# Kernel tuning notes

Measured on AMD Instinct MI355X. Metric: run time of the kernel, lower is better.

Reference implementation:

```python
import jax, jax.numpy as jnp
import numpy as np

N_FEATURES = 4096
N_GROUPS = 1024
BATCH = 8192


def _make_groups():
    # Deterministic variable-size groups: size_g = 2 + (g % 7), sizes in [2, 8].
    rng = np.random.RandomState(0)
    sizes = 2 + (np.arange(N_GROUPS) % 7)
    flat_idx = rng.randint(0, N_FEATURES, size=int(sizes.sum())).astype(np.int64)
    seg_ids = np.repeat(np.arange(N_GROUPS, dtype=np.int64), sizes)
    return flat_idx, seg_ids


def setup_inputs() -> dict:
    key = jax.random.key(0)
    k1, k2, k3, k4 = jax.random.split(key, 4)
    flat_idx_np, seg_ids_np = _make_groups()
    total = flat_idx_np.shape[0]  # 5115
    x = jax.random.normal(k1, (BATCH, N_FEATURES), dtype=jnp.float32)
    # Concatenated per-group HeNormal-style weights (shape (size,1) flattened).
    w_flat = jax.random.normal(k2, (total,), dtype=jnp.float32)
    # SimplyConnected weight (Ones init in original; random here for testing).
    diag_w = jax.random.uniform(k3, (N_GROUPS,), dtype=jnp.float32)
    # Dense kernel [n_groups, units=1], no bias.
    dense_W = jax.random.normal(k4, (N_GROUPS, 1), dtype=jnp.float32) * (2.0 / N_GROUPS) ** 0.5
    return {
        "x": x,
        "flat_idx": jnp.asarray(flat_idx_np),
        "seg_ids": jnp.asarray(seg_ids_np),
        "w_flat": w_flat,
        "diag_w": diag_w,
        "dense_W": dense_W,
    }


def reference(x, flat_idx, seg_ids, w_flat, diag_w, dense_W):
    # GroupConnected: per-group gather + (size,1) matmul == segmented weighted sum.
    # gathered: [B, total_idx]; weighted then segment-summed over groups -> [B, n_groups]
    weighted = x[:, flat_idx] * w_flat  # [B, total]
    grouped = jax.ops.segment_sum(weighted.T, seg_ids, num_segments=N_GROUPS).T  # [B, G]
    # diagblock (depth-2 = 1 SimplyConnected): elementwise scale, then Dense (no bias).
    return (grouped * diag_w) @ dense_W  # [B, units=1]
```

## Files before the change

kernel.cpp:

```cpp
#include <hip/hip_runtime.h>

#define N_FEATURES 4096
#define N_GROUPS   1024
#define BATCH      8192
#define NV4        (N_FEATURES / 4)

__global__ __launch_bounds__(1024) void build_coeff_kernel(
    const int* __restrict__ flat_idx,
    const int* __restrict__ seg_ids,
    const float* __restrict__ w_flat,
    const float* __restrict__ diag_w,
    const float* __restrict__ dense_W,
    float* __restrict__ coeff,
    int total)
{
    __shared__ float s_coeff[N_FEATURES];
    for (int i = threadIdx.x; i < N_FEATURES; i += blockDim.x) s_coeff[i] = 0.0f;
    __syncthreads();
    for (int i = threadIdx.x; i < total; i += blockDim.x) {
        int g = seg_ids[i];
        float c = w_flat[i] * diag_w[g] * dense_W[g];
        atomicAdd(&s_coeff[flat_idx[i]], c);
    }
    __syncthreads();
    for (int i = threadIdx.x; i < N_FEATURES; i += blockDim.x) coeff[i] = s_coeff[i];
}

__global__ __launch_bounds__(256) void gemv_kernel(
    const float* __restrict__ x,
    const float* __restrict__ coeff,
    float* __restrict__ out)
{
    __shared__ float4 s_c[NV4];
    const float4* __restrict__ c4 = (const float4*)coeff;
    for (int i = threadIdx.x; i < NV4; i += 256) s_c[i] = c4[i];
    __syncthreads();

    const int wid  = threadIdx.x >> 6;
    const int lane = threadIdx.x & 63;
    const int row  = (blockIdx.x << 2) + wid;

    const float4* __restrict__ xr = (const float4*)(x + (size_t)row * N_FEATURES);

    float acc = 0.0f;
#pragma unroll
    for (int k = 0; k < 16; ++k) {
        const int i = (k << 6) + lane;
        float4 xv = xr[i];
        float4 cv = s_c[i];
        acc += xv.x * cv.x + xv.y * cv.y + xv.z * cv.z + xv.w * cv.w;
    }

#pragma unroll
    for (int off = 32; off > 0; off >>= 1)
        acc += __shfl_down(acc, off, 64);

    if (lane == 0)
        out[row] = acc;
}

extern "C" void kernel_launch(void* const* d_in, const int* in_sizes, int n_in,
                              void* d_out, int out_size, void* d_ws, size_t ws_size,
                              hipStream_t stream) {
    const float* x        = (const float*)d_in[0];
    const int*   flat_idx = (const int*)d_in[1];
    const int*   seg_ids  = (const int*)d_in[2];
    const float* w_flat   = (const float*)d_in[3];
    const float* diag_w   = (const float*)d_in[4];
    const float* dense_W  = (const float*)d_in[5];
    float* out = (float*)d_out;
    const int total = in_sizes[1];

    float* coeff = (float*)d_ws;

    build_coeff_kernel<<<1, 1024, 0, stream>>>(flat_idx, seg_ids, w_flat,
                                               diag_w, dense_W, coeff, total);
    gemv_kernel<<<BATCH / 4, 256, 0, stream>>>(x, coeff, out);
}
```

Before: 206.5 us.

## Fuse coefficient build into GEMV and prefetch x rows before building

```diff
diff --git a/kernel.cpp b/kernel.cpp
--- a/kernel.cpp
+++ b/kernel.cpp
@@ -5,50 +5,43 @@
 #define BATCH      8192
 #define NV4        (N_FEATURES / 4)
 
-__global__ __launch_bounds__(1024) void build_coeff_kernel(
+__global__ __launch_bounds__(256) void fused_kernel(
+    const float* __restrict__ x,
     const int* __restrict__ flat_idx,
     const int* __restrict__ seg_ids,
     const float* __restrict__ w_flat,
     const float* __restrict__ diag_w,
     const float* __restrict__ dense_W,
-    float* __restrict__ coeff,
+    float* __restrict__ out,
     int total)
 {
     __shared__ float s_coeff[N_FEATURES];
-    for (int i = threadIdx.x; i < N_FEATURES; i += blockDim.x) s_coeff[i] = 0.0f;
-    __syncthreads();
-    for (int i = threadIdx.x; i < total; i += blockDim.x) {
-        int g = seg_ids[i];
-        float c = w_flat[i] * diag_w[g] * dense_W[g];
-        atomicAdd(&s_coeff[flat_idx[i]], c);
-    }
-    __syncthreads();
-    for (int i = threadIdx.x; i < N_FEATURES; i += blockDim.x) coeff[i] = s_coeff[i];
-}
-
-__global__ __launch_bounds__(256) void gemv_kernel(
-    const float* __restrict__ x,
-    const float* __restrict__ coeff,
-    float* __restrict__ out)
-{
-    __shared__ float4 s_c[NV4];
-    const float4* __restrict__ c4 = (const float4*)coeff;
-    for (int i = threadIdx.x; i < NV4; i += 256) s_c[i] = c4[i];
-    __syncthreads();
 
     const int wid  = threadIdx.x >> 6;
     const int lane = threadIdx.x & 63;
     const int row  = (blockIdx.x << 2) + wid;
 
     const float4* __restrict__ xr = (const float4*)(x + (size_t)row * N_FEATURES);
+    float4 xv[16];
+#pragma unroll
+    for (int k = 0; k < 16; ++k)
+        xv[k] = xr[(k << 6) + lane];
 
+    for (int i = threadIdx.x; i < N_FEATURES; i += 256) s_coeff[i] = 0.0f;
+    __syncthreads();
+    for (int i = threadIdx.x; i < total; i += 256) {
+        int g = seg_ids[i];
+        float c = w_flat[i] * diag_w[g] * dense_W[g];
+        atomicAdd(&s_coeff[flat_idx[i]], c);
+    }
+    __syncthreads();
+
+    const float4* sc = (const float4*)s_coeff;
     float acc = 0.0f;
 #pragma unroll
     for (int k = 0; k < 16; ++k) {
-        const int i = (k << 6) + lane;
-        float4 xv = xr[i];
-        float4 cv = s_c[i];
-        acc += xv.x * cv.x + xv.y * cv.y + xv.z * cv.z + xv.w * cv.w;
+        float4 cv = sc[(k << 6) + lane];
+        acc += xv[k].x * cv.x + xv[k].y * cv.y + xv[k].z * cv.z + xv[k].w * cv.w;
     }
 
 #pragma unroll
@@ -71,9 +64,6 @@
     float* out = (float*)d_out;
     const int total = in_sizes[1];
 
-    float* coeff = (float*)d_ws;
-
-    build_coeff_kernel<<<1, 1024, 0, stream>>>(flat_idx, seg_ids, w_flat,
-                                               diag_w, dense_W, coeff, total);
-    gemv_kernel<<<BATCH / 4, 256, 0, stream>>>(x, coeff, out);
+    fused_kernel<<<BATCH / 4, 256, 0, stream>>>(x, flat_idx, seg_ids, w_flat,
+                                                diag_w, dense_W, out, total);
 }
```

Result: slower. 244.1 us (+18.2%).
